# Kernel optimization log

Hardware: AMD Instinct MI355X
Metric: run time of the kernel (lower is better)

The kernel has to match this reference:

```python
import jax, jax.numpy as jnp
import numpy as np
from jax import lax

BATCH = 8192
HIDDEN = 128
N_POINTS = 8
MAX_STEPS = 8     # adaptive substep budget per output interval
RTOL, ATOL = 1e-3, 1e-4

# Dormand-Prince 5(4) tableau (FSAL)
A21 = 1/5
A31, A32 = 3/40, 9/40
A41, A42, A43 = 44/45, -56/15, 32/9
A51, A52, A53, A54 = 19372/6561, -25360/2187, 64448/6561, -212/729
A61, A62, A63, A64, A65 = 9017/3168, -355/33, 46732/5247, 49/176, -5103/18656
B1, B3, B4, B5, B6 = 35/384, 500/1113, 125/192, -2187/6784, 11/84
# error weights = b(5th) - b(4th)
E1 = 35/384 - 5179/57600
E3 = 500/1113 - 7571/16695
E4 = 125/192 - 393/640
E5 = -2187/6784 + 92097/339200
E6 = 11/84 - 187/2100
E7 = -1/40


def setup_inputs() -> dict:
    key = jax.random.key(0)
    ks = jax.random.split(key, 6)
    def xavier(k, fi, fo):
        return (jax.random.normal(k, (fi, fo)) * jnp.sqrt(2.0 / (fi + fo))).astype(jnp.float32)
    W1 = xavier(ks[0], 2, HIDDEN); b1 = jnp.zeros((HIDDEN,), jnp.float32)
    W2 = xavier(ks[1], HIDDEN, HIDDEN); b2 = jnp.zeros((HIDDEN,), jnp.float32)
    W3 = xavier(ks[2], HIDDEN, HIDDEN); b3 = jnp.zeros((HIDDEN,), jnp.float32)
    W4 = xavier(ks[3], HIDDEN, 2); b4 = jnp.zeros((2,), jnp.float32)
    x0 = jax.random.normal(ks[4], (BATCH, 2), jnp.float32)
    t = (jnp.arange(N_POINTS, dtype=jnp.float32) * 0.1)
    return {"x0": x0, "t": t, "W1": W1, "b1": b1, "W2": W2, "b2": b2,
            "W3": W3, "b3": b3, "W4": W4, "b4": b4}


def _odeint(x0, t, W1, b1, W2, b2, W3, b3, W4, b4):
    def f(y):  # autonomous dynamics: ODEFunc ignores t
        h = jax.nn.elu(y @ W1 + b1)
        h = jax.nn.elu(h @ W2 + b2)
        h = jax.nn.elu(h @ W3 + b3)
        return h @ W4 + b4

    def dopri5_step(y, h):
        k1 = f(y)
        k2 = f(y + h * (A21 * k1))
        k3 = f(y + h * (A31 * k1 + A32 * k2))
        k4 = f(y + h * (A41 * k1 + A42 * k2 + A43 * k3))
        k5 = f(y + h * (A51 * k1 + A52 * k2 + A53 * k3 + A54 * k4))
        k6 = f(y + h * (A61 * k1 + A62 * k2 + A63 * k3 + A64 * k4 + A65 * k5))
        y5 = y + h * (B1 * k1 + B3 * k3 + B4 * k4 + B5 * k5 + B6 * k6)
        k7 = f(y5)  # FSAL stage, used only for error estimate here
        err = h * (E1 * k1 + E3 * k3 + E4 * k4 + E5 * k5 + E6 * k6 + E7 * k7)
        tol = ATOL + RTOL * jnp.maximum(jnp.abs(y), jnp.abs(y5))
        err_norm = jnp.sqrt(jnp.mean((err / tol) ** 2))
        return y5, err_norm

    def solve_interval(carry, ts):
        y, h = carry
        t0, t1 = ts

        def body(c, _):
            y, tc, h = c
            remaining = t1 - tc
            done = remaining <= 1e-9
            h_eff = jnp.where(done, h, jnp.minimum(h, remaining))
            y5, err_norm = dopri5_step(y, h_eff)
            accept = (err_norm <= 1.0) & (~done)
            y = jnp.where(accept, y5, y)
            tc = jnp.where(accept, tc + h_eff, tc)
            factor = jnp.clip(0.9 * jnp.maximum(err_norm, 1e-10) ** (-0.2), 0.2, 10.0)
            h = jnp.where(done, h, h_eff * factor)
            return (y, tc, h), None

        (y, _, h), _ = lax.scan(body, (y, t0, h), None, length=MAX_STEPS)
        return (y, h), y

    h0 = (t[1] - t[0]) * 0.5
    (_, _), ys = lax.scan(solve_interval, (x0, h0), (t[:-1], t[1:]))
    return jnp.concatenate([x0[None], ys], axis=0)  # (n_points, batch, 2)


def reference(x0, t, W1, b1, W2, b2, W3, b3, W4, b4):
    return _odeint(x0, t, W1, b1, W2, b2, W3, b3, W4, b4)
```

## Files before the change

kernel.cpp:

```cpp
#include <hip/hip_runtime.h>
#include <stdint.h>

typedef unsigned int u32;
typedef unsigned short u16;
typedef float f32x4 __attribute__((ext_vector_type(4)));
typedef float f32x2 __attribute__((ext_vector_type(2)));
typedef short short8 __attribute__((ext_vector_type(8)));
typedef unsigned short ushort8 __attribute__((ext_vector_type(8)));
typedef unsigned int u32x2 __attribute__((ext_vector_type(2)));
typedef unsigned int u32x4 __attribute__((ext_vector_type(4)));

#define HID  128
#define MT   32
#define NWG  256
#define NTHR 512
#define LD   136

#define OFF_PART  0
#define OFF_CNT   2048
#define OFF_WPACK 4096
#define OFF_W2TH  8192
#define OFF_W2TL  40960
#define OFF_W3TH  73728
#define OFF_W3TL  106496

constexpr float CA21 = (float)(1.0/5.0);
constexpr float CA31 = (float)(3.0/40.0),   CA32 = (float)(9.0/40.0);
constexpr float CA41 = (float)(44.0/45.0),  CA42 = (float)(-56.0/15.0), CA43 = (float)(32.0/9.0);
constexpr float CA51 = (float)(19372.0/6561.0), CA52 = (float)(-25360.0/2187.0);
constexpr float CA53 = (float)(64448.0/6561.0), CA54 = (float)(-212.0/729.0);
constexpr float CA61 = (float)(9017.0/3168.0),  CA62 = (float)(-355.0/33.0);
constexpr float CA63 = (float)(46732.0/5247.0), CA64 = (float)(49.0/176.0), CA65 = (float)(-5103.0/18656.0);
constexpr float CB1 = (float)(35.0/384.0), CB3 = (float)(500.0/1113.0), CB4 = (float)(125.0/192.0);
constexpr float CB5 = (float)(-2187.0/6784.0), CB6 = (float)(11.0/84.0);
constexpr float CE1 = (float)(35.0/384.0 - 5179.0/57600.0);
constexpr float CE3 = (float)(500.0/1113.0 - 7571.0/16695.0);
constexpr float CE4 = (float)(125.0/192.0 - 393.0/640.0);
constexpr float CE5 = (float)(-2187.0/6784.0 + 92097.0/339200.0);
constexpr float CE6 = (float)(11.0/84.0 - 187.0/2100.0);
constexpr float CE7 = (float)(-1.0/40.0);

template<int N> struct IC { static constexpr int v = N; };

__device__ __forceinline__ u16 f2bf(float x) {
  u32 u = __builtin_bit_cast(u32, x);
  u32 r = (u + 0x7FFFu + ((u >> 16) & 1u)) >> 16;
  return (u16)r;
}
__device__ __forceinline__ float bf2f(u16 b) {
  u32 u = ((u32)b) << 16;
  return __builtin_bit_cast(float, u);
}
__device__ __forceinline__ float eluf(float x) {
  return x > 0.f ? x : (__expf(x) - 1.f);
}
__device__ __forceinline__ u32 cvtpk(float a, float b) {
  u32 r; asm("v_cvt_pk_bf16_f32 %0, %1, %2" : "=v"(r) : "v"(a), "v"(b)); return r;
}

__global__ void prologue(const float* __restrict__ x0, const float* __restrict__ t,
                         const float* __restrict__ W1, const float* __restrict__ b1,
                         const float* __restrict__ W2, const float* __restrict__ b2,
                         const float* __restrict__ W3, const float* __restrict__ b3,
                         const float* __restrict__ W4, const float* __restrict__ b4,
                         float* __restrict__ ws, float* __restrict__ out)
{
  int gid = blockIdx.x * blockDim.x + threadIdx.x;
  out[gid] = x0[gid];
  {
    int k = gid >> 7, j = gid & 127;
    u16* w2th = (u16*)((char*)ws + OFF_W2TH);
    u16* w2tl = (u16*)((char*)ws + OFF_W2TL);
    u16* w3th = (u16*)((char*)ws + OFF_W3TH);
    u16* w3tl = (u16*)((char*)ws + OFF_W3TL);
    float w = W2[gid];
    u16 hb = f2bf(w);
    w2th[j*HID + k] = hb;
    w2tl[j*HID + k] = f2bf(w - bf2f(hb));
    w = W3[gid];
    hb = f2bf(w);
    w3th[j*HID + k] = hb;
    w3tl[j*HID + k] = f2bf(w - bf2f(hb));
  }
  float* wp = ws + OFF_WPACK/4;
  if (gid < 256) wp[gid] = W1[gid];
  if (gid < 128) {
    wp[256 + gid] = b1[gid];
    wp[384 + gid] = b2[gid];
    wp[512 + gid] = b3[gid];
  }
  if (gid < 2)  wp[640 + gid] = b4[gid];
  if (gid < 64) ((u32*)((char*)ws + OFF_CNT))[gid] = 0u;
}

__global__ __launch_bounds__(NTHR, 2)
void solver(const float* __restrict__ x0, const float* __restrict__ t_arr,
            const float* __restrict__ W4g, float* __restrict__ ws,
            float* __restrict__ out)
{
  const int tid  = threadIdx.x;
  const int wg   = blockIdx.x;
  const int lane = tid & 63;
  const int wv   = tid >> 6;
  const int nl   = lane & 15;
  const int g    = lane >> 4;

  __shared__ __align__(16) u16 Ahi[2][MT][LD];
  __shared__ __align__(16) u16 Alo[2][MT][LD];
  __shared__ __align__(16) float Wsm[644];
  __shared__ float kS[7][MT][2];
  __shared__ float yL[MT][2];
  __shared__ float y5L[MT][2];
  __shared__ float pD[8][2][16][2];
  __shared__ float red[8];

  {
    const float* wp = ws + OFF_WPACK/4;
    Wsm[tid] = wp[tid];
    if (tid < 132) Wsm[512 + tid] = wp[512 + tid];
  }
  if (tid < 64) yL[tid >> 1][tid & 1] = x0[wg*64 + tid];

  const u16* w2th = (const u16*)((const char*)ws + OFF_W2TH);
  const u16* w2tl = (const u16*)((const char*)ws + OFF_W2TL);
  const u16* w3th = (const u16*)((const char*)ws + OFF_W3TH);
  const u16* w3tl = (const u16*)((const char*)ws + OFF_W3TL);
  short8 W2H[4], W2L[4], W3H[4], W3L[4];
  {
    const int nglob = wv*16 + nl;
#pragma unroll
    for (int ks = 0; ks < 4; ++ks) {
      int off = nglob*HID + ks*32 + g*8;
      W2H[ks] = *(const short8*)(w2th + off);
      W2L[ks] = *(const short8*)(w2tl + off);
      W3H[ks] = *(const short8*)(w3th + off);
      W3L[ks] = *(const short8*)(w3tl + off);
    }
  }
  float w4c[4][2];
#pragma unroll
  for (int r = 0; r < 4; ++r) {
    int n = wv*16 + g*4 + r;
    w4c[r][0] = W4g[n*2 + 0];
    w4c[r][1] = W4g[n*2 + 1];
  }
  __syncthreads();
  const f32x4 bv2 = *(const f32x4*)&Wsm[384 + wv*16 + g*4];
  const f32x4 bv3 = *(const f32x4*)&Wsm[512 + wv*16 + g*4];

  float* part = (float*)((char*)ws + OFF_PART);
  u32*  cnt   = (u32*) ((char*)ws + OFF_CNT);

  float h = 0.5f * (t_arr[1] - t_arr[0]);
  float heff = h;

  auto phaseA = [&](auto SC, int fromPD) {
    constexpr int S = decltype(SC)::v;
    const int m  = tid >> 4;
    const int jc = tid & 15;
    float ys0, ys1;
    const float y0 = yL[m][0], y1 = yL[m][1];
    if constexpr (S == 1) {
      ys0 = y0; ys1 = y1;
    } else {
      const int mt = m >> 4, ml = m & 15;
      float kp0, kp1;
      if (S == 2 && !fromPD) {
        kp0 = kS[0][m][0]; kp1 = kS[0][m][1];
      } else {
        kp0 = Wsm[640]; kp1 = Wsm[641];
#pragma unroll
        for (int w = 0; w < 8; ++w) {
          f32x2 p = *(const f32x2*)&pD[w][mt][ml][0];
          kp0 += p[0]; kp1 += p[1];
        }
        if (jc < 2) kS[S-2][m][jc] = jc ? kp1 : kp0;
      }
      if constexpr (S == 2) {
        ys0 = fmaf(heff, CA21*kp0, y0);
        ys1 = fmaf(heff, CA21*kp1, y1);
      } else if constexpr (S == 3) {
        f32x2 k1 = *(const f32x2*)&kS[0][m][0];
        ys0 = fmaf(heff, CA31*k1[0] + CA32*kp0, y0);
        ys1 = fmaf(heff, CA31*k1[1] + CA32*kp1, y1);
      } else if constexpr (S == 4) {
        f32x2 k1 = *(const f32x2*)&kS[0][m][0];
        f32x2 k2 = *(const f32x2*)&kS[1][m][0];
        ys0 = fmaf(heff, CA41*k1[0] + CA42*k2[0] + CA43*kp0, y0);
        ys1 = fmaf(heff, CA41*k1[1] + CA42*k2[1] + CA43*kp1, y1);
      } else if constexpr (S == 5) {
        f32x2 k1 = *(const f32x2*)&kS[0][m][0];
        f32x2 k2 = *(const f32x2*)&kS[1][m][0];
        f32x2 k3 = *(const f32x2*)&kS[2][m][0];
        ys0 = fmaf(heff, CA51*k1[0] + CA52*k2[0] + CA53*k3[0] + CA54*kp0, y0);
        ys1 = fmaf(heff, CA51*k1[1] + CA52*k2[1] + CA53*k3[1] + CA54*kp1, y1);
      } else if constexpr (S == 6) {
        f32x2 k1 = *(const f32x2*)&kS[0][m][0];
        f32x2 k2 = *(const f32x2*)&kS[1][m][0];
        f32x2 k3 = *(const f32x2*)&kS[2][m][0];
        f32x2 k4 = *(const f32x2*)&kS[3][m][0];
        ys0 = fmaf(heff, CA61*k1[0] + CA62*k2[0] + CA63*k3[0] + CA64*k4[0] + CA65*kp0, y0);
        ys1 = fmaf(heff, CA61*k1[1] + CA62*k2[1] + CA63*k3[1] + CA64*k4[1] + CA65*kp1, y1);
      } else {
        f32x2 k1 = *(const f32x2*)&kS[0][m][0];
        f32x2 k3 = *(const f32x2*)&kS[2][m][0];
        f32x2 k4 = *(const f32x2*)&kS[3][m][0];
        f32x2 k5 = *(const f32x2*)&kS[4][m][0];
        ys0 = fmaf(heff, CB1*k1[0] + CB3*k3[0] + CB4*k4[0] + CB5*k5[0] + CB6*kp0, y0);
        ys1 = fmaf(heff, CB1*k1[1] + CB3*k3[1] + CB4*k4[1] + CB5*k5[1] + CB6*kp1, y1);
        if (jc < 2) y5L[m][jc] = jc ? ys1 : ys0;
      }
    }
    const int j0 = jc * 8;
    f32x4 w0a = *(const f32x4*)&Wsm[j0],        w0b = *(const f32x4*)&Wsm[j0 + 4];
    f32x4 w1a = *(const f32x4*)&Wsm[128 + j0],  w1b = *(const f32x4*)&Wsm[128 + j0 + 4];
    f32x4 ba  = *(const f32x4*)&Wsm[256 + j0],  bb  = *(const f32x4*)&Wsm[256 + j0 + 4];
    float v[8];
#pragma unroll
    for (int jj = 0; jj < 4; ++jj)
      v[jj] = eluf(fmaf(ys1, w1a[jj], fmaf(ys0, w0a[jj], ba[jj])));
#pragma unroll
    for (int jj = 0; jj < 4; ++jj)
      v[4+jj] = eluf(fmaf(ys1, w1b[jj], fmaf(ys0, w0b[jj], bb[jj])));
    u32 h01 = cvtpk(v[0], v[1]), h23 = cvtpk(v[2], v[3]);
    u32 h45 = cvtpk(v[4], v[5]), h67 = cvtpk(v[6], v[7]);
    float l0 = v[0] - __builtin_bit_cast(float, h01 << 16);
    float l1 = v[1] - __builtin_bit_cast(float, h01 & 0xffff0000u);
    float l2 = v[2] - __builtin_bit_cast(float, h23 << 16);
    float l3 = v[3] - __builtin_bit_cast(float, h23 & 0xffff0000u);
    float l4 = v[4] - __builtin_bit_cast(float, h45 << 16);
    float l5 = v[5] - __builtin_bit_cast(float, h45 & 0xffff0000u);
    float l6 = v[6] - __builtin_bit_cast(float, h67 << 16);
    float l7 = v[7] - __builtin_bit_cast(float, h67 & 0xffff0000u);
    u32x4 hp = {h01, h23, h45, h67};
    u32x4 lp = {cvtpk(l0,l1), cvtpk(l2,l3), cvtpk(l4,l5), cvtpk(l6,l7)};
    *(u32x4*)&Ahi[0][m][j0] = hp;
    *(u32x4*)&Alo[0][m][j0] = lp;
  };

  auto mmL2 = [&]() {
    f32x4 a0[2], a1[2], a2[2];
#pragma unroll
    for (int mt = 0; mt < 2; ++mt) { a0[mt] = bv2; a1[mt] = {0,0,0,0}; a2[mt] = {0,0,0,0}; }
#pragma unroll
    for (int ks = 0; ks < 4; ++ks) {
#pragma unroll
      for (int mt = 0; mt < 2; ++mt) {
        short8 bh = *(const short8*)&Ahi[0][mt*16 + nl][ks*32 + g*8];
        short8 bl = *(const short8*)&Alo[0][mt*16 + nl][ks*32 + g*8];
        a0[mt] = __builtin_amdgcn_mfma_f32_16x16x32_bf16(W2H[ks], bh, a0[mt], 0, 0, 0);
        a1[mt] = __builtin_amdgcn_mfma_f32_16x16x32_bf16(W2L[ks], bh, a1[mt], 0, 0, 0);
        a2[mt] = __builtin_amdgcn_mfma_f32_16x16x32_bf16(W2H[ks], bl, a2[mt], 0, 0, 0);
      }
    }
    const int n0 = wv*16 + g*4;
#pragma unroll
    for (int mt = 0; mt < 2; ++mt) {
      float v0 = eluf(a0[mt][0] + a1[mt][0] + a2[mt][0]);
      float v1 = eluf(a0[mt][1] + a1[mt][1] + a2[mt][1]);
      float v2 = eluf(a0[mt][2] + a1[mt][2] + a2[mt][2]);
      float v3 = eluf(a0[mt][3] + a1[mt][3] + a2[mt][3]);
      u32 h01 = cvtpk(v0, v1), h23 = cvtpk(v2, v3);
      float l0 = v0 - __builtin_bit_cast(float, h01 << 16);
      float l1 = v1 - __builtin_bit_cast(float, h01 & 0xffff0000u);
      float l2 = v2 - __builtin_bit_cast(float, h23 << 16);
      float l3 = v3 - __builtin_bit_cast(float, h23 & 0xffff0000u);
      u32x2 hp = {h01, h23};
      u32x2 lp = {cvtpk(l0,l1), cvtpk(l2,l3)};
      *(u32x2*)&Ahi[1][mt*16 + nl][n0] = hp;
      *(u32x2*)&Alo[1][mt*16 + nl][n0] = lp;
    }
  };

  auto mmL3 = [&]() {
    f32x4 a0[2], a1[2], a2[2];
#pragma unroll
    for (int mt = 0; mt < 2; ++mt) { a0[mt] = bv3; a1[mt] = {0,0,0,0}; a2[mt] = {0,0,0,0}; }
#pragma unroll
    for (int ks = 0; ks < 4; ++ks) {
#pragma unroll
      for (int mt = 0; mt < 2; ++mt) {
        short8 bh = *(const short8*)&Ahi[1][mt*16 + nl][ks*32 + g*8];
        short8 bl = *(const short8*)&Alo[1][mt*16 + nl][ks*32 + g*8];
        a0[mt] = __builtin_amdgcn_mfma_f32_16x16x32_bf16(W3H[ks], bh, a0[mt], 0, 0, 0);
        a1[mt] = __builtin_amdgcn_mfma_f32_16x16x32_bf16(W3L[ks], bh, a1[mt], 0, 0, 0);
        a2[mt] = __builtin_amdgcn_mfma_f32_16x16x32_bf16(W3H[ks], bl, a2[mt], 0, 0, 0);
      }
    }
#pragma unroll
    for (int mt = 0; mt < 2; ++mt) {
      float v0 = eluf(a0[mt][0] + a1[mt][0] + a2[mt][0]);
      float v1 = eluf(a0[mt][1] + a1[mt][1] + a2[mt][1]);
      float v2 = eluf(a0[mt][2] + a1[mt][2] + a2[mt][2]);
      float v3 = eluf(a0[mt][3] + a1[mt][3] + a2[mt][3]);
      float p0 = v0*w4c[0][0] + v1*w4c[1][0] + v2*w4c[2][0] + v3*w4c[3][0];
      float p1 = v0*w4c[0][1] + v1*w4c[1][1] + v2*w4c[2][1] + v3*w4c[3][1];
      p0 += __shfl_xor(p0, 16); p0 += __shfl_xor(p0, 32);
      p1 += __shfl_xor(p1, 16); p1 += __shfl_xor(p1, 32);
      if (lane < 16) {
        f32x2 pp = {p0, p1};
        *(f32x2*)&pD[wv][mt][lane][0] = pp;
      }
    }
  };

  for (int iv = 0; iv < 7; ++iv) {
    const float t1 = t_arr[iv + 1];
    float tc = t_arr[iv];
    for (int s = 0; s < 8; ++s) {
      const int step = iv*8 + s;
      float rem = t1 - tc;
      if (rem <= 1e-9f) break;
      heff = fminf(h, rem);

      if (iv == 0 && s == 0) {
        phaseA(IC<1>{}, 0); __syncthreads();
        mmL2(); __syncthreads();
        mmL3(); __syncthreads();
        phaseA(IC<2>{}, 1);
      } else {
        phaseA(IC<2>{}, 0);
      }
      __syncthreads(); mmL2(); __syncthreads(); mmL3(); __syncthreads();
      phaseA(IC<3>{}, 1); __syncthreads(); mmL2(); __syncthreads(); mmL3(); __syncthreads();
      phaseA(IC<4>{}, 1); __syncthreads(); mmL2(); __syncthreads(); mmL3(); __syncthreads();
      phaseA(IC<5>{}, 1); __syncthreads(); mmL2(); __syncthreads(); mmL3(); __syncthreads();
      phaseA(IC<6>{}, 1); __syncthreads(); mmL2(); __syncthreads(); mmL3(); __syncthreads();
      phaseA(IC<7>{}, 1); __syncthreads(); mmL2(); __syncthreads(); mmL3(); __syncthreads();

      if (wv == 0) {
        int m = lane >> 1, c = lane & 1;
        int emt = m >> 4, eml = m & 15;
        float kp = Wsm[640 + c];
#pragma unroll
        for (int w = 0; w < 8; ++w) kp += pD[w][emt][eml][c];
        kS[6][m][c] = kp;
        float e = heff * (CE1*kS[0][m][c] + CE3*kS[2][m][c] + CE4*kS[3][m][c]
                        + CE5*kS[4][m][c] + CE6*kS[5][m][c] + CE7*kp);
        float tol = 1e-4f + 1e-3f * fmaxf(fabsf(yL[m][c]), fabsf(y5L[m][c]));
        float rr = e / tol;
        float es = rr * rr;
#pragma unroll
        for (int mk = 1; mk < 64; mk <<= 1) es += __shfl_xor(es, mk);
        if (lane == 0) {
          __hip_atomic_store(&part[(step & 1)*256 + wg], es, __ATOMIC_RELAXED, __HIP_MEMORY_SCOPE_AGENT);
          __hip_atomic_fetch_add(&cnt[step], 1u, __ATOMIC_RELEASE, __HIP_MEMORY_SCOPE_AGENT);
        }
      }
      if (tid == 0) {
        while (__hip_atomic_load(&cnt[step], __ATOMIC_ACQUIRE, __HIP_MEMORY_SCOPE_AGENT) < (u32)NWG)
          __builtin_amdgcn_s_sleep(2);
      }
      __syncthreads();
      float pv = 0.f;
      if (tid < 256)
        pv = __hip_atomic_load(&part[(step & 1)*256 + tid], __ATOMIC_RELAXED, __HIP_MEMORY_SCOPE_AGENT);
#pragma unroll
      for (int mk = 1; mk < 64; mk <<= 1) pv += __shfl_xor(pv, mk);
      if (tid < 256 && lane == 0) red[wv] = pv;
      __syncthreads();
      float err_norm = sqrtf((red[0] + red[1] + red[2] + red[3]) * (1.0f/16384.f));
      bool acc = (err_norm <= 1.0f);
      float factor = fminf(10.f, fmaxf(0.2f, 0.9f * powf(fmaxf(err_norm, 1e-10f), -0.2f)));
      if (acc) {
        if (tid < 64) { int m = tid >> 1, c = tid & 1;
          yL[m][c] = y5L[m][c];
          kS[0][m][c] = kS[6][m][c];
        }
        tc += heff;
      }
      h = heff * factor;
      __syncthreads();
    }
    if (tid < 64)
      out[(size_t)(iv + 1) * 16384 + wg*64 + tid] = yL[tid >> 1][tid & 1];
  }
}

extern "C" void kernel_launch(void* const* d_in, const int* in_sizes, int n_in,
                              void* d_out, int out_size, void* d_ws, size_t ws_size,
                              hipStream_t stream)
{
  const float* x0 = (const float*)d_in[0];
  const float* t  = (const float*)d_in[1];
  const float* W1 = (const float*)d_in[2];
  const float* b1 = (const float*)d_in[3];
  const float* W2 = (const float*)d_in[4];
  const float* b2 = (const float*)d_in[5];
  const float* W3 = (const float*)d_in[6];
  const float* b3 = (const float*)d_in[7];
  const float* W4 = (const float*)d_in[8];
  const float* b4 = (const float*)d_in[9];
  float* out = (float*)d_out;
  float* ws  = (float*)d_ws;

  prologue<<<64, 256, 0, stream>>>(x0, t, W1, b1, W2, b2, W3, b3, W4, b4, ws, out);
  solver<<<NWG, NTHR, 0, stream>>>(x0, t, W4, ws, out);
}
```

Measured before the change: 198.8 us.

## Halve rows per workgroup to 16 and launch 512 workgroups

```diff
diff --git a/kernel.cpp b/kernel.cpp
--- a/kernel.cpp
+++ b/kernel.cpp
@@ -11,18 +11,18 @@
 typedef unsigned int u32x4 __attribute__((ext_vector_type(4)));
 
 #define HID  128
-#define MT   32
-#define NWG  256
+#define MT   16
+#define NWG  512
 #define NTHR 512
 #define LD   136
 
 #define OFF_PART  0
-#define OFF_CNT   2048
-#define OFF_WPACK 4096
-#define OFF_W2TH  8192
-#define OFF_W2TL  40960
-#define OFF_W3TH  73728
-#define OFF_W3TL  106496
+#define OFF_CNT   4096
+#define OFF_WPACK 8192
+#define OFF_W2TH  16384
+#define OFF_W2TL  49152
+#define OFF_W3TH  81920
+#define OFF_W3TL  114688
 
 constexpr float CA21 = (float)(1.0/5.0);
 constexpr float CA31 = (float)(3.0/40.0),   CA32 = (float)(9.0/40.0);
@@ -93,7 +93,7 @@
   if (gid < 64) ((u32*)((char*)ws + OFF_CNT))[gid] = 0u;
 }
 
-__global__ __launch_bounds__(NTHR, 2)
+__global__ __launch_bounds__(NTHR, 4)
 void solver(const float* __restrict__ x0, const float* __restrict__ t_arr,
             const float* __restrict__ W4g, float* __restrict__ ws,
             float* __restrict__ out)
@@ -108,10 +108,10 @@
   __shared__ __align__(16) u16 Ahi[2][MT][LD];
   __shared__ __align__(16) u16 Alo[2][MT][LD];
   __shared__ __align__(16) float Wsm[644];
-  __shared__ float kS[7][MT][2];
-  __shared__ float yL[MT][2];
-  __shared__ float y5L[MT][2];
-  __shared__ float pD[8][2][16][2];
+  __shared__ __align__(16) float kS[7][MT][2];
+  __shared__ __align__(16) float yL[MT][2];
+  __shared__ __align__(16) float y5L[MT][2];
+  __shared__ __align__(16) float pD[8][MT][2];
   __shared__ float red[8];
 
   {
@@ -119,7 +119,7 @@
     Wsm[tid] = wp[tid];
     if (tid < 132) Wsm[512 + tid] = wp[512 + tid];
   }
-  if (tid < 64) yL[tid >> 1][tid & 1] = x0[wg*64 + tid];
+  if (tid < 32) yL[tid >> 1][tid & 1] = x0[wg*32 + tid];
 
   const u16* w2th = (const u16*)((const char*)ws + OFF_W2TH);
   const u16* w2tl = (const u16*)((const char*)ws + OFF_W2TL);
@@ -148,22 +148,21 @@
   const f32x4 bv2 = *(const f32x4*)&Wsm[384 + wv*16 + g*4];
   const f32x4 bv3 = *(const f32x4*)&Wsm[512 + wv*16 + g*4];
 
-  float* part = (float*)((char*)ws + OFF_PART);
-  u32*  cnt   = (u32*) ((char*)ws + OFF_CNT);
+  float* part = ws + OFF_PART/4;
+  u32*  cnt   = (u32*)((char*)ws + OFF_CNT);
 
   float h = 0.5f * (t_arr[1] - t_arr[0]);
   float heff = h;
 
   auto phaseA = [&](auto SC, int fromPD) {
     constexpr int S = decltype(SC)::v;
-    const int m  = tid >> 4;
-    const int jc = tid & 15;
+    const int m  = tid >> 5;
+    const int jc = tid & 31;
     float ys0, ys1;
     const float y0 = yL[m][0], y1 = yL[m][1];
     if constexpr (S == 1) {
       ys0 = y0; ys1 = y1;
     } else {
-      const int mt = m >> 4, ml = m & 15;
       float kp0, kp1;
       if (S == 2 && !fromPD) {
         kp0 = kS[0][m][0]; kp1 = kS[0][m][1];
@@ -171,7 +170,7 @@
         kp0 = Wsm[640]; kp1 = Wsm[641];
 #pragma unroll
         for (int w = 0; w < 8; ++w) {
-          f32x2 p = *(const f32x2*)&pD[w][mt][ml][0];
+          f32x2 p = *(const f32x2*)&pD[w][m][0];
           kp0 += p[0]; kp1 += p[1];
         }
         if (jc < 2) kS[S-2][m][jc] = jc ? kp1 : kp0;
@@ -211,96 +210,76 @@
         if (jc < 2) y5L[m][jc] = jc ? ys1 : ys0;
       }
     }
-    const int j0 = jc * 8;
-    f32x4 w0a = *(const f32x4*)&Wsm[j0],        w0b = *(const f32x4*)&Wsm[j0 + 4];
-    f32x4 w1a = *(const f32x4*)&Wsm[128 + j0],  w1b = *(const f32x4*)&Wsm[128 + j0 + 4];
-    f32x4 ba  = *(const f32x4*)&Wsm[256 + j0],  bb  = *(const f32x4*)&Wsm[256 + j0 + 4];
-    float v[8];
-#pragma unroll
-    for (int jj = 0; jj < 4; ++jj)
-      v[jj] = eluf(fmaf(ys1, w1a[jj], fmaf(ys0, w0a[jj], ba[jj])));
-#pragma unroll
-    for (int jj = 0; jj < 4; ++jj)
-      v[4+jj] = eluf(fmaf(ys1, w1b[jj], fmaf(ys0, w0b[jj], bb[jj])));
-    u32 h01 = cvtpk(v[0], v[1]), h23 = cvtpk(v[2], v[3]);
-    u32 h45 = cvtpk(v[4], v[5]), h67 = cvtpk(v[6], v[7]);
-    float l0 = v[0] - __builtin_bit_cast(float, h01 << 16);
-    float l1 = v[1] - __builtin_bit_cast(float, h01 & 0xffff0000u);
-    float l2 = v[2] - __builtin_bit_cast(float, h23 << 16);
-    float l3 = v[3] - __builtin_bit_cast(float, h23 & 0xffff0000u);
-    float l4 = v[4] - __builtin_bit_cast(float, h45 << 16);
-    float l5 = v[5] - __builtin_bit_cast(float, h45 & 0xffff0000u);
-    float l6 = v[6] - __builtin_bit_cast(float, h67 << 16);
-    float l7 = v[7] - __builtin_bit_cast(float, h67 & 0xffff0000u);
-    u32x4 hp = {h01, h23, h45, h67};
-    u32x4 lp = {cvtpk(l0,l1), cvtpk(l2,l3), cvtpk(l4,l5), cvtpk(l6,l7)};
-    *(u32x4*)&Ahi[0][m][j0] = hp;
-    *(u32x4*)&Alo[0][m][j0] = lp;
+    const int j0 = jc * 4;
+    f32x4 w0 = *(const f32x4*)&Wsm[j0];
+    f32x4 w1 = *(const f32x4*)&Wsm[128 + j0];
+    f32x4 bb = *(const f32x4*)&Wsm[256 + j0];
+    float v0 = eluf(fmaf(ys1, w1[0], fmaf(ys0, w0[0], bb[0])));
+    float v1 = eluf(fmaf(ys1, w1[1], fmaf(ys0, w0[1], bb[1])));
+    float v2 = eluf(fmaf(ys1, w1[2], fmaf(ys0, w0[2], bb[2])));
+    float v3 = eluf(fmaf(ys1, w1[3], fmaf(ys0, w0[3], bb[3])));
+    u32 h01 = cvtpk(v0, v1), h23 = cvtpk(v2, v3);
+    float l0 = v0 - __builtin_bit_cast(float, h01 << 16);
+    float l1 = v1 - __builtin_bit_cast(float, h01 & 0xffff0000u);
+    float l2 = v2 - __builtin_bit_cast(float, h23 << 16);
+    float l3 = v3 - __builtin_bit_cast(float, h23 & 0xffff0000u);
+    u32x2 hp = {h01, h23};
+    u32x2 lp = {cvtpk(l0, l1), cvtpk(l2, l3)};
+    *(u32x2*)&Ahi[0][m][j0] = hp;
+    *(u32x2*)&Alo[0][m][j0] = lp;
   };
 
   auto mmL2 = [&]() {
-    f32x4 a0[2], a1[2], a2[2];
-#pragma unroll
-    for (int mt = 0; mt < 2; ++mt) { a0[mt] = bv2; a1[mt] = {0,0,0,0}; a2[mt] = {0,0,0,0}; }
+    f32x4 a0 = bv2, a1 = {0,0,0,0}, a2 = {0,0,0,0};
+    __builtin_amdgcn_s_setprio(1);
 #pragma unroll
     for (int ks = 0; ks < 4; ++ks) {
-#pragma unroll
-      for (int mt = 0; mt < 2; ++mt) {
-        short8 bh = *(const short8*)&Ahi[0][mt*16 + nl][ks*32 + g*8];
-        short8 bl = *(const short8*)&Alo[0][mt*16 + nl][ks*32 + g*8];
-        a0[mt] = __builtin_amdgcn_mfma_f32_16x16x32_bf16(W2H[ks], bh, a0[mt], 0, 0, 0);
-        a1[mt] = __builtin_amdgcn_mfma_f32_16x16x32_bf16(W2L[ks], bh, a1[mt], 0, 0, 0);
-        a2[mt] = __builtin_amdgcn_mfma_f32_16x16x32_bf16(W2H[ks], bl, a2[mt], 0, 0, 0);
-      }
-    }
+      short8 bh = *(const short8*)&Ahi[0][nl][ks*32 + g*8];
+      short8 bl = *(const short8*)&Alo[0][nl][ks*32 + g*8];
+      a0 = __builtin_amdgcn_mfma_f32_16x16x32_bf16(W2H[ks], bh, a0, 0, 0, 0);
+      a1 = __builtin_amdgcn_mfma_f32_16x16x32_bf16(W2L[ks], bh, a1, 0, 0, 0);
+      a2 = __builtin_amdgcn_mfma_f32_16x16x32_bf16(W2H[ks], bl, a2, 0, 0, 0);
+    }
+    __builtin_amdgcn_s_setprio(0);
+    float v0 = eluf(a0[0] + a1[0] + a2[0]);
+    float v1 = eluf(a0[1] + a1[1] + a2[1]);
+    float v2 = eluf(a0[2] + a1[2] + a2[2]);
+    float v3 = eluf(a0[3] + a1[3] + a2[3]);
+    u32 h01 = cvtpk(v0, v1), h23 = cvtpk(v2, v3);
+    float l0 = v0 - __builtin_bit_cast(float, h01 << 16);
+    float l1 = v1 - __builtin_bit_cast(float, h01 & 0xffff0000u);
+    float l2 = v2 - __builtin_bit_cast(float, h23 << 16);
+    float l3 = v3 - __builtin_bit_cast(float, h23 & 0xffff0000u);
+    u32x2 hp = {h01, h23};
+    u32x2 lp = {cvtpk(l0, l1), cvtpk(l2, l3)};
     const int n0 = wv*16 + g*4;
-#pragma unroll
-    for (int mt = 0; mt < 2; ++mt) {
-      float v0 = eluf(a0[mt][0] + a1[mt][0] + a2[mt][0]);
-      float v1 = eluf(a0[mt][1] + a1[mt][1] + a2[mt][1]);
-      float v2 = eluf(a0[mt][2] + a1[mt][2] + a2[mt][2]);
-      float v3 = eluf(a0[mt][3] + a1[mt][3] + a2[mt][3]);
-      u32 h01 = cvtpk(v0, v1), h23 = cvtpk(v2, v3);
-      float l0 = v0 - __builtin_bit_cast(float, h01 << 16);
-      float l1 = v1 - __builtin_bit_cast(float, h01 & 0xffff0000u);
-      float l2 = v2 - __builtin_bit_cast(float, h23 << 16);
-      float l3 = v3 - __builtin_bit_cast(float, h23 & 0xffff0000u);
-      u32x2 hp = {h01, h23};
-      u32x2 lp = {cvtpk(l0,l1), cvtpk(l2,l3)};
-      *(u32x2*)&Ahi[1][mt*16 + nl][n0] = hp;
-      *(u32x2*)&Alo[1][mt*16 + nl][n0] = lp;
-    }
+    *(u32x2*)&Ahi[1][nl][n0] = hp;
+    *(u32x2*)&Alo[1][nl][n0] = lp;
   };
 
   auto mmL3 = [&]() {
-    f32x4 a0[2], a1[2], a2[2];
-#pragma unroll
-    for (int mt = 0; mt < 2; ++mt) { a0[mt] = bv3; a1[mt] = {0,0,0,0}; a2[mt] = {0,0,0,0}; }
+    f32x4 a0 = bv3, a1 = {0,0,0,0}, a2 = {0,0,0,0};
+    __builtin_amdgcn_s_setprio(1);
 #pragma unroll
     for (int ks = 0; ks < 4; ++ks) {
-#pragma unroll
-      for (int mt = 0; mt < 2; ++mt) {
-        short8 bh = *(const short8*)&Ahi[1][mt*16 + nl][ks*32 + g*8];
-        short8 bl = *(const short8*)&Alo[1][mt*16 + nl][ks*32 + g*8];
-        a0[mt] = __builtin_amdgcn_mfma_f32_16x16x32_bf16(W3H[ks], bh, a0[mt], 0, 0, 0);
-        a1[mt] = __builtin_amdgcn_mfma_f32_16x16x32_bf16(W3L[ks], bh, a1[mt], 0, 0, 0);
-        a2[mt] = __builtin_amdgcn_mfma_f32_16x16x32_bf16(W3H[ks], bl, a2[mt], 0, 0, 0);
-      }
-    }
-#pragma unroll
-    for (int mt = 0; mt < 2; ++mt) {
-      float v0 = eluf(a0[mt][0] + a1[mt][0] + a2[mt][0]);
-      float v1 = eluf(a0[mt][1] + a1[mt][1] + a2[mt][1]);
-      float v2 = eluf(a0[mt][2] + a1[mt][2] + a2[mt][2]);
-      float v3 = eluf(a0[mt][3] + a1[mt][3] + a2[mt][3]);
-      float p0 = v0*w4c[0][0] + v1*w4c[1][0] + v2*w4c[2][0] + v3*w4c[3][0];
-      float p1 = v0*w4c[0][1] + v1*w4c[1][1] + v2*w4c[2][1] + v3*w4c[3][1];
-      p0 += __shfl_xor(p0, 16); p0 += __shfl_xor(p0, 32);
-      p1 += __shfl_xor(p1, 16); p1 += __shfl_xor(p1, 32);
-      if (lane < 16) {
-        f32x2 pp = {p0, p1};
-        *(f32x2*)&pD[wv][mt][lane][0] = pp;
-      }
+      short8 bh = *(const short8*)&Ahi[1][nl][ks*32 + g*8];
+      short8 bl = *(const short8*)&Alo[1][nl][ks*32 + g*8];
+      a0 = __builtin_amdgcn_mfma_f32_16x16x32_bf16(W3H[ks], bh, a0, 0, 0, 0);
+      a1 = __builtin_amdgcn_mfma_f32_16x16x32_bf16(W3L[ks], bh, a1, 0, 0, 0);
+      a2 = __builtin_amdgcn_mfma_f32_16x16x32_bf16(W3H[ks], bl, a2, 0, 0, 0);
+    }
+    __builtin_amdgcn_s_setprio(0);
+    float v0 = eluf(a0[0] + a1[0] + a2[0]);
+    float v1 = eluf(a0[1] + a1[1] + a2[1]);
+    float v2 = eluf(a0[2] + a1[2] + a2[2]);
+    float v3 = eluf(a0[3] + a1[3] + a2[3]);
+    float p0 = v0*w4c[0][0] + v1*w4c[1][0] + v2*w4c[2][0] + v3*w4c[3][0];
+    float p1 = v0*w4c[0][1] + v1*w4c[1][1] + v2*w4c[2][1] + v3*w4c[3][1];
+    p0 += __shfl_xor(p0, 16); p0 += __shfl_xor(p0, 32);
+    p1 += __shfl_xor(p1, 16); p1 += __shfl_xor(p1, 32);
+    if (lane < 16) {
+      f32x2 pp = {p0, p1};
+      *(f32x2*)&pD[wv][lane][0] = pp;
     }
   };
 
@@ -328,12 +307,11 @@
       phaseA(IC<6>{}, 1); __syncthreads(); mmL2(); __syncthreads(); mmL3(); __syncthreads();
       phaseA(IC<7>{}, 1); __syncthreads(); mmL2(); __syncthreads(); mmL3(); __syncthreads();
 
-      if (wv == 0) {
+      if (wv == 0 && lane < 32) {
         int m = lane >> 1, c = lane & 1;
-        int emt = m >> 4, eml = m & 15;
         float kp = Wsm[640 + c];
 #pragma unroll
-        for (int w = 0; w < 8; ++w) kp += pD[w][emt][eml][c];
+        for (int w = 0; w < 8; ++w) kp += pD[w][m][c];
         kS[6][m][c] = kp;
         float e = heff * (CE1*kS[0][m][c] + CE3*kS[2][m][c] + CE4*kS[3][m][c]
                         + CE5*kS[4][m][c] + CE6*kS[5][m][c] + CE7*kp);
@@ -341,9 +319,9 @@
         float rr = e / tol;
         float es = rr * rr;
 #pragma unroll
-        for (int mk = 1; mk < 64; mk <<= 1) es += __shfl_xor(es, mk);
+        for (int mk = 1; mk < 32; mk <<= 1) es += __shfl_xor(es, mk);
         if (lane == 0) {
-          __hip_atomic_store(&part[(step & 1)*256 + wg], es, __ATOMIC_RELAXED, __HIP_MEMORY_SCOPE_AGENT);
+          __hip_atomic_store(&part[(step & 1)*NWG + wg], es, __ATOMIC_RELAXED, __HIP_MEMORY_SCOPE_AGENT);
           __hip_atomic_fetch_add(&cnt[step], 1u, __ATOMIC_RELEASE, __HIP_MEMORY_SCOPE_AGENT);
         }
       }
@@ -352,18 +330,17 @@
           __builtin_amdgcn_s_sleep(2);
       }
       __syncthreads();
-      float pv = 0.f;
-      if (tid < 256)
-        pv = __hip_atomic_load(&part[(step & 1)*256 + tid], __ATOMIC_RELAXED, __HIP_MEMORY_SCOPE_AGENT);
+      float pv = __hip_atomic_load(&part[(step & 1)*NWG + tid], __ATOMIC_RELAXED, __HIP_MEMORY_SCOPE_AGENT);
 #pragma unroll
       for (int mk = 1; mk < 64; mk <<= 1) pv += __shfl_xor(pv, mk);
-      if (tid < 256 && lane == 0) red[wv] = pv;
+      if (lane == 0) red[wv] = pv;
       __syncthreads();
-      float err_norm = sqrtf((red[0] + red[1] + red[2] + red[3]) * (1.0f/16384.f));
+      float err_norm = sqrtf((red[0] + red[1] + red[2] + red[3]
+                            + red[4] + red[5] + red[6] + red[7]) * (1.0f/16384.f));
       bool acc = (err_norm <= 1.0f);
       float factor = fminf(10.f, fmaxf(0.2f, 0.9f * powf(fmaxf(err_norm, 1e-10f), -0.2f)));
       if (acc) {
-        if (tid < 64) { int m = tid >> 1, c = tid & 1;
+        if (tid < 32) { int m = tid >> 1, c = tid & 1;
           yL[m][c] = y5L[m][c];
           kS[0][m][c] = kS[6][m][c];
         }
@@ -372,8 +349,8 @@
       h = heff * factor;
       __syncthreads();
     }
-    if (tid < 64)
-      out[(size_t)(iv + 1) * 16384 + wg*64 + tid] = yL[tid >> 1][tid & 1];
+    if (tid < 32)
+      out[(size_t)(iv + 1) * 16384 + wg*32 + tid] = yL[tid >> 1][tid & 1];
   }
 }
 
```

Result: slower. 443.6 us (+123.2%).

## Drop activation low-part split, add priority hints, and use tree-based grid reduction

Applied to the files above, without the earlier changes.

```diff
diff --git a/kernel.cpp b/kernel.cpp
--- a/kernel.cpp
+++ b/kernel.cpp
@@ -6,7 +6,6 @@
 typedef float f32x4 __attribute__((ext_vector_type(4)));
 typedef float f32x2 __attribute__((ext_vector_type(2)));
 typedef short short8 __attribute__((ext_vector_type(8)));
-typedef unsigned short ushort8 __attribute__((ext_vector_type(8)));
 typedef unsigned int u32x2 __attribute__((ext_vector_type(2)));
 typedef unsigned int u32x4 __attribute__((ext_vector_type(4)));
 
@@ -17,12 +16,15 @@
 #define LD   136
 
 #define OFF_PART  0
-#define OFF_CNT   2048
-#define OFF_WPACK 4096
-#define OFF_W2TH  8192
-#define OFF_W2TL  40960
-#define OFF_W3TH  73728
-#define OFF_W3TL  106496
+#define OFF_LEAF  2048
+#define OFF_ROOT  5632
+#define OFF_FLAG  5888
+#define OFF_HPAY  6144
+#define OFF_WPACK 8192
+#define OFF_W2TH  16384
+#define OFF_W2TL  49152
+#define OFF_W3TH  81920
+#define OFF_W3TL  114688
 
 constexpr float CA21 = (float)(1.0/5.0);
 constexpr float CA31 = (float)(3.0/40.0),   CA32 = (float)(9.0/40.0);
@@ -90,7 +92,7 @@
     wp[512 + gid] = b3[gid];
   }
   if (gid < 2)  wp[640 + gid] = b4[gid];
-  if (gid < 64) ((u32*)((char*)ws + OFF_CNT))[gid] = 0u;
+  if (gid < 1600) ((u32*)ws)[gid] = 0u;
 }
 
 __global__ __launch_bounds__(NTHR, 2)
@@ -106,13 +108,14 @@
   const int g    = lane >> 4;
 
   __shared__ __align__(16) u16 Ahi[2][MT][LD];
-  __shared__ __align__(16) u16 Alo[2][MT][LD];
   __shared__ __align__(16) float Wsm[644];
-  __shared__ float kS[7][MT][2];
-  __shared__ float yL[MT][2];
-  __shared__ float y5L[MT][2];
-  __shared__ float pD[8][2][16][2];
+  __shared__ __align__(16) float kS[7][MT][2];
+  __shared__ __align__(16) float yL[MT][2];
+  __shared__ __align__(16) float y5L[MT][2];
+  __shared__ __align__(16) float pD[8][2][16][2];
   __shared__ float red[8];
+  __shared__ u32 bcF;
+  __shared__ float bcH;
 
   {
     const float* wp = ws + OFF_WPACK/4;
@@ -148,8 +151,11 @@
   const f32x4 bv2 = *(const f32x4*)&Wsm[384 + wv*16 + g*4];
   const f32x4 bv3 = *(const f32x4*)&Wsm[512 + wv*16 + g*4];
 
-  float* part = (float*)((char*)ws + OFF_PART);
-  u32*  cnt   = (u32*) ((char*)ws + OFF_CNT);
+  float* part = ws + OFF_PART/4;
+  u32*  leaf  = (u32*)((char*)ws + OFF_LEAF);
+  u32*  root  = (u32*)((char*)ws + OFF_ROOT);
+  u32*  flg   = (u32*)((char*)ws + OFF_FLAG);
+  float* hpay = (float*)((char*)ws + OFF_HPAY);
 
   float h = 0.5f * (t_arr[1] - t_arr[0]);
   float heff = h;
@@ -212,87 +218,66 @@
       }
     }
     const int j0 = jc * 8;
-    f32x4 w0a = *(const f32x4*)&Wsm[j0],        w0b = *(const f32x4*)&Wsm[j0 + 4];
-    f32x4 w1a = *(const f32x4*)&Wsm[128 + j0],  w1b = *(const f32x4*)&Wsm[128 + j0 + 4];
-    f32x4 ba  = *(const f32x4*)&Wsm[256 + j0],  bb  = *(const f32x4*)&Wsm[256 + j0 + 4];
-    float v[8];
-#pragma unroll
-    for (int jj = 0; jj < 4; ++jj)
-      v[jj] = eluf(fmaf(ys1, w1a[jj], fmaf(ys0, w0a[jj], ba[jj])));
-#pragma unroll
-    for (int jj = 0; jj < 4; ++jj)
-      v[4+jj] = eluf(fmaf(ys1, w1b[jj], fmaf(ys0, w0b[jj], bb[jj])));
-    u32 h01 = cvtpk(v[0], v[1]), h23 = cvtpk(v[2], v[3]);
-    u32 h45 = cvtpk(v[4], v[5]), h67 = cvtpk(v[6], v[7]);
-    float l0 = v[0] - __builtin_bit_cast(float, h01 << 16);
-    float l1 = v[1] - __builtin_bit_cast(float, h01 & 0xffff0000u);
-    float l2 = v[2] - __builtin_bit_cast(float, h23 << 16);
-    float l3 = v[3] - __builtin_bit_cast(float, h23 & 0xffff0000u);
-    float l4 = v[4] - __builtin_bit_cast(float, h45 << 16);
-    float l5 = v[5] - __builtin_bit_cast(float, h45 & 0xffff0000u);
-    float l6 = v[6] - __builtin_bit_cast(float, h67 << 16);
-    float l7 = v[7] - __builtin_bit_cast(float, h67 & 0xffff0000u);
-    u32x4 hp = {h01, h23, h45, h67};
-    u32x4 lp = {cvtpk(l0,l1), cvtpk(l2,l3), cvtpk(l4,l5), cvtpk(l6,l7)};
+    f32x4 w0a = *(const f32x4*)&Wsm[j0],       w0b = *(const f32x4*)&Wsm[j0 + 4];
+    f32x4 w1a = *(const f32x4*)&Wsm[128 + j0], w1b = *(const f32x4*)&Wsm[128 + j0 + 4];
+    f32x4 ba  = *(const f32x4*)&Wsm[256 + j0], bb  = *(const f32x4*)&Wsm[256 + j0 + 4];
+    float v0 = eluf(fmaf(ys1, w1a[0], fmaf(ys0, w0a[0], ba[0])));
+    float v1 = eluf(fmaf(ys1, w1a[1], fmaf(ys0, w0a[1], ba[1])));
+    float v2 = eluf(fmaf(ys1, w1a[2], fmaf(ys0, w0a[2], ba[2])));
+    float v3 = eluf(fmaf(ys1, w1a[3], fmaf(ys0, w0a[3], ba[3])));
+    float v4 = eluf(fmaf(ys1, w1b[0], fmaf(ys0, w0b[0], bb[0])));
+    float v5 = eluf(fmaf(ys1, w1b[1], fmaf(ys0, w0b[1], bb[1])));
+    float v6 = eluf(fmaf(ys1, w1b[2], fmaf(ys0, w0b[2], bb[2])));
+    float v7 = eluf(fmaf(ys1, w1b[3], fmaf(ys0, w0b[3], bb[3])));
+    u32x4 hp = {cvtpk(v0,v1), cvtpk(v2,v3), cvtpk(v4,v5), cvtpk(v6,v7)};
     *(u32x4*)&Ahi[0][m][j0] = hp;
-    *(u32x4*)&Alo[0][m][j0] = lp;
   };
 
   auto mmL2 = [&]() {
-    f32x4 a0[2], a1[2], a2[2];
-#pragma unroll
-    for (int mt = 0; mt < 2; ++mt) { a0[mt] = bv2; a1[mt] = {0,0,0,0}; a2[mt] = {0,0,0,0}; }
-#pragma unroll
-    for (int ks = 0; ks < 4; ++ks) {
+    f32x4 a0[2], a1[2];
+    a0[0] = bv2; a0[1] = bv2; a1[0] = {0,0,0,0}; a1[1] = {0,0,0,0};
+    __builtin_amdgcn_s_setprio(1);
+#pragma unroll
+    for (int ks = 0; ks < 4; ++ks)
 #pragma unroll
       for (int mt = 0; mt < 2; ++mt) {
         short8 bh = *(const short8*)&Ahi[0][mt*16 + nl][ks*32 + g*8];
-        short8 bl = *(const short8*)&Alo[0][mt*16 + nl][ks*32 + g*8];
         a0[mt] = __builtin_amdgcn_mfma_f32_16x16x32_bf16(W2H[ks], bh, a0[mt], 0, 0, 0);
         a1[mt] = __builtin_amdgcn_mfma_f32_16x16x32_bf16(W2L[ks], bh, a1[mt], 0, 0, 0);
-        a2[mt] = __builtin_amdgcn_mfma_f32_16x16x32_bf16(W2H[ks], bl, a2[mt], 0, 0, 0);
-      }
-    }
+      }
+    __builtin_amdgcn_s_setprio(0);
     const int n0 = wv*16 + g*4;
 #pragma unroll
     for (int mt = 0; mt < 2; ++mt) {
-      float v0 = eluf(a0[mt][0] + a1[mt][0] + a2[mt][0]);
-      float v1 = eluf(a0[mt][1] + a1[mt][1] + a2[mt][1]);
-      float v2 = eluf(a0[mt][2] + a1[mt][2] + a2[mt][2]);
-      float v3 = eluf(a0[mt][3] + a1[mt][3] + a2[mt][3]);
-      u32 h01 = cvtpk(v0, v1), h23 = cvtpk(v2, v3);
-      float l0 = v0 - __builtin_bit_cast(float, h01 << 16);
-      float l1 = v1 - __builtin_bit_cast(float, h01 & 0xffff0000u);
-      float l2 = v2 - __builtin_bit_cast(float, h23 << 16);
-      float l3 = v3 - __builtin_bit_cast(float, h23 & 0xffff0000u);
-      u32x2 hp = {h01, h23};
-      u32x2 lp = {cvtpk(l0,l1), cvtpk(l2,l3)};
+      float v0 = eluf(a0[mt][0] + a1[mt][0]);
+      float v1 = eluf(a0[mt][1] + a1[mt][1]);
+      float v2 = eluf(a0[mt][2] + a1[mt][2]);
+      float v3 = eluf(a0[mt][3] + a1[mt][3]);
+      u32x2 hp = {cvtpk(v0, v1), cvtpk(v2, v3)};
       *(u32x2*)&Ahi[1][mt*16 + nl][n0] = hp;
-      *(u32x2*)&Alo[1][mt*16 + nl][n0] = lp;
     }
   };
 
   auto mmL3 = [&]() {
-    f32x4 a0[2], a1[2], a2[2];
-#pragma unroll
-    for (int mt = 0; mt < 2; ++mt) { a0[mt] = bv3; a1[mt] = {0,0,0,0}; a2[mt] = {0,0,0,0}; }
-#pragma unroll
-    for (int ks = 0; ks < 4; ++ks) {
+    f32x4 a0[2], a1[2];
+    a0[0] = bv3; a0[1] = bv3; a1[0] = {0,0,0,0}; a1[1] = {0,0,0,0};
+    __builtin_amdgcn_s_setprio(1);
+#pragma unroll
+    for (int ks = 0; ks < 4; ++ks)
 #pragma unroll
       for (int mt = 0; mt < 2; ++mt) {
         short8 bh = *(const short8*)&Ahi[1][mt*16 + nl][ks*32 + g*8];
-        short8 bl = *(const short8*)&Alo[1][mt*16 + nl][ks*32 + g*8];
         a0[mt] = __builtin_amdgcn_mfma_f32_16x16x32_bf16(W3H[ks], bh, a0[mt], 0, 0, 0);
         a1[mt] = __builtin_amdgcn_mfma_f32_16x16x32_bf16(W3L[ks], bh, a1[mt], 0, 0, 0);
-        a2[mt] = __builtin_amdgcn_mfma_f32_16x16x32_bf16(W3H[ks], bl, a2[mt], 0, 0, 0);
-      }
-    }
+      }
+    __builtin_amdgcn_s_setprio(0);
 #pragma unroll
     for (int mt = 0; mt < 2; ++mt) {
-      float v0 = eluf(a0[mt][0] + a1[mt][0] + a2[mt][0]);
-      float v1 = eluf(a0[mt][1] + a1[mt][1] + a2[mt][1]);
-      float v2 = eluf(a0[mt][2] + a1[mt][2] + a2[mt][2]);
-      float v3 = eluf(a0[mt][3] + a1[mt][3] + a2[mt][3]);
+      float v0 = a0[mt][0] + a1[mt][0];
+      float v1 = a0[mt][1] + a1[mt][1];
+      float v2 = a0[mt][2] + a1[mt][2];
+      float v3 = a0[mt][3] + a1[mt][3];
+      v0 = eluf(v0); v1 = eluf(v1); v2 = eluf(v2); v3 = eluf(v3);
       float p0 = v0*w4c[0][0] + v1*w4c[1][0] + v2*w4c[2][0] + v3*w4c[3][0];
       float p1 = v0*w4c[0][1] + v1*w4c[1][1] + v2*w4c[2][1] + v3*w4c[3][1];
       p0 += __shfl_xor(p0, 16); p0 += __shfl_xor(p0, 32);
@@ -343,33 +328,52 @@
 #pragma unroll
         for (int mk = 1; mk < 64; mk <<= 1) es += __shfl_xor(es, mk);
         if (lane == 0) {
-          __hip_atomic_store(&part[(step & 1)*256 + wg], es, __ATOMIC_RELAXED, __HIP_MEMORY_SCOPE_AGENT);
-          __hip_atomic_fetch_add(&cnt[step], 1u, __ATOMIC_RELEASE, __HIP_MEMORY_SCOPE_AGENT);
+          __hip_atomic_store(&part[(step & 1)*NWG + wg], es, __ATOMIC_RELAXED, __HIP_MEMORY_SCOPE_AGENT);
+          u32 old = __hip_atomic_fetch_add(&leaf[step*16 + (wg >> 4)], 1u, __ATOMIC_ACQ_REL, __HIP_MEMORY_SCOPE_AGENT);
+          if (old == 15u)
+            __hip_atomic_fetch_add(&root[step], 1u, __ATOMIC_ACQ_REL, __HIP_MEMORY_SCOPE_AGENT);
         }
       }
+      if (wg == 0) {
+        if (tid == 0) {
+          while (__hip_atomic_load(&root[step], __ATOMIC_ACQUIRE, __HIP_MEMORY_SCOPE_AGENT) < 16u)
+            __builtin_amdgcn_s_sleep(2);
+        }
+        __syncthreads();
+        float pv = 0.f;
+        if (tid < NWG)
+          pv = __hip_atomic_load(&part[(step & 1)*NWG + tid], __ATOMIC_RELAXED, __HIP_MEMORY_SCOPE_AGENT);
+#pragma unroll
+        for (int mk = 1; mk < 64; mk <<= 1) pv += __shfl_xor(pv, mk);
+        if (lane == 0) red[wv] = pv;
+        __syncthreads();
+        if (tid == 0) {
+          float err_norm = sqrtf((red[0] + red[1] + red[2] + red[3]) * (1.0f/16384.f));
+          bool acc = (err_norm <= 1.0f);
+          float factor = fminf(10.f, fmaxf(0.2f, 0.9f * powf(fmaxf(err_norm, 1e-10f), -0.2f)));
+          __hip_atomic_store(&hpay[step], heff * factor, __ATOMIC_RELAXED, __HIP_MEMORY_SCOPE_AGENT);
+          __hip_atomic_store(&flg[step], acc ? 3u : 1u, __ATOMIC_RELEASE, __HIP_MEMORY_SCOPE_AGENT);
+        }
+      }
       if (tid == 0) {
-        while (__hip_atomic_load(&cnt[step], __ATOMIC_ACQUIRE, __HIP_MEMORY_SCOPE_AGENT) < (u32)NWG)
+        u32 f;
+        while (((f = __hip_atomic_load(&flg[step], __ATOMIC_ACQUIRE, __HIP_MEMORY_SCOPE_AGENT)) & 1u) == 0u)
           __builtin_amdgcn_s_sleep(2);
+        bcF = f;
+        bcH = __hip_atomic_load(&hpay[step], __ATOMIC_RELAXED, __HIP_MEMORY_SCOPE_AGENT);
       }
       __syncthreads();
-      float pv = 0.f;
-      if (tid < 256)
-        pv = __hip_atomic_load(&part[(step & 1)*256 + tid], __ATOMIC_RELAXED, __HIP_MEMORY_SCOPE_AGENT);
-#pragma unroll
-      for (int mk = 1; mk < 64; mk <<= 1) pv += __shfl_xor(pv, mk);
-      if (tid < 256 && lane == 0) red[wv] = pv;
-      __syncthreads();
-      float err_norm = sqrtf((red[0] + red[1] + red[2] + red[3]) * (1.0f/16384.f));
-      bool acc = (err_norm <= 1.0f);
-      float factor = fminf(10.f, fmaxf(0.2f, 0.9f * powf(fmaxf(err_norm, 1e-10f), -0.2f)));
-      if (acc) {
-        if (tid < 64) { int m = tid >> 1, c = tid & 1;
-          yL[m][c] = y5L[m][c];
-          kS[0][m][c] = kS[6][m][c];
+      {
+        bool acc = (bcF & 2u) != 0u;
+        if (acc) {
+          if (tid < 64) { int m = tid >> 1, c = tid & 1;
+            yL[m][c] = y5L[m][c];
+            kS[0][m][c] = kS[6][m][c];
+          }
+          tc += heff;
         }
-        tc += heff;
-      }
-      h = heff * factor;
+        h = bcH;
+      }
       __syncthreads();
     }
     if (tid < 64)
```

Result: slower. 256.5 us (+29.0%).
